# Kernel tuning notes

Measured on AMD Instinct MI355X. Metric: run time of the kernel, lower is better.

## Reference

```python
import jax, jax.numpy as jnp
import numpy as np

N = 50000          # nodes
E = 1600000        # edges (before self-loops)
DIN = 128
HEADS = (8, 8, 4)
FEATS = (16, 16, 16)
NEG_SLOPE = 0.2


def setup_inputs() -> dict:
    key = jax.random.key(0)
    ks = jax.random.split(key, 2 + 4 * 3)
    inp = {
        "X": jax.random.normal(ks[0], (N, DIN), dtype=jnp.float32),
        "A": jax.random.randint(ks[1], (2, E), 0, N, dtype=jnp.int32),
    }
    in_dims = [DIN, HEADS[0] * FEATS[0], HEADS[1] * FEATS[1]]
    k = 2
    for i, (h, f) in enumerate(zip(HEADS, FEATS)):
        din = in_dims[i]
        concat = i + 1 < len(HEADS)
        inp[f"W{i+1}"] = jax.random.normal(ks[k], (din, h * f), dtype=jnp.float32) / np.float32(np.sqrt(din)); k += 1
        inp[f"as{i+1}"] = jax.random.normal(ks[k], (h, f), dtype=jnp.float32) * 0.1; k += 1
        inp[f"ad{i+1}"] = jax.random.normal(ks[k], (h, f), dtype=jnp.float32) * 0.1; k += 1
        inp[f"b{i+1}"] = jnp.zeros((h * f if concat else f,), dtype=jnp.float32); k += 1
    return inp


def _gat_conv(x, src, dst, W, a_src, a_dst, b, concat):
    # PyG-style GATConv (eval mode, self-loops already in src/dst)
    H, F = a_src.shape
    h = (x @ W).reshape(-1, H, F)                     # [N, H, F]
    e = jax.nn.leaky_relu((h * a_src).sum(-1)[src] + (h * a_dst).sum(-1)[dst], NEG_SLOPE)  # [Etot, H]
    m = jax.ops.segment_max(e, dst, num_segments=N)   # segment softmax over dst neighborhoods
    ex = jnp.exp(e - m[dst])
    s = jax.ops.segment_sum(ex, dst, num_segments=N)
    alpha = ex / (s[dst] + 1e-16)                     # [Etot, H]
    out = jax.ops.segment_sum(h[src] * alpha[:, :, None], dst, num_segments=N)  # [N, H, F]
    out = out.reshape(N, H * F) if concat else out.mean(axis=1)
    return out + b


def reference(X, A, W1, as1, ad1, b1, W2, as2, ad2, b2, W3, as3, ad3, b3):
    loops = jnp.arange(N, dtype=A.dtype)              # GATConv default add_self_loops=True
    src = jnp.concatenate([A[0], loops])
    dst = jnp.concatenate([A[1], loops])
    x = jax.nn.relu(_gat_conv(X, src, dst, W1, as1, ad1, b1, True))
    x = jax.nn.relu(_gat_conv(x, src, dst, W2, as2, ad2, b2, True))
    return _gat_conv(x, src, dst, W3, as3, ad3, b3, False)
```

## Files before the change

kernel.cpp:

```cpp
#include <hip/hip_runtime.h>
#include <hip/hip_bf16.h>

#define NN 50000
#define EE 1600000
#define DIN 128

#define BKT_SHIFT 6
#define NB ((NN + 63) >> 6)
#define BSLACK 2688
#define CHUNK 4096

typedef _Float16 half_t;
typedef __attribute__((ext_vector_type(2))) _Float16 half2_t;
typedef __attribute__((ext_vector_type(4))) _Float16 half4_t;
typedef __attribute__((ext_vector_type(8))) _Float16 half8_t;
typedef __attribute__((ext_vector_type(4))) float float4_t;

__device__ __forceinline__ void split_write(half_t* __restrict__ bh, half_t* __restrict__ bl,
                                            int idx, float v) {
    half_t h = (half_t)v;
    bh[idx] = h;
    bl[idx] = (half_t)(v - (float)h);
}

__device__ __forceinline__ void build_bt(const float* __restrict__ W,
                                         const float* __restrict__ as,
                                         const float* __restrict__ ad,
                                         half_t* __restrict__ Bh, half_t* __restrict__ Bl,
                                         int elem, int NCOL, int H) {
    int r = elem >> 7, k = elem & 127;
    float v;
    if (r < NCOL) {
        v = W[k * NCOL + r];
    } else {
        int j = r - NCOL;
        v = 0.f;
        if (j < 8) {
            if (j < H) {
                float s = 0.f;
#pragma unroll
                for (int f = 0; f < 16; ++f) s += W[k * NCOL + j * 16 + f] * as[j * 16 + f];
                v = s;
            }
        } else {
            int hh = j - 8;
            if (hh < H) {
                float s = 0.f;
#pragma unroll
                for (int f = 0; f < 16; ++f) s += W[k * NCOL + hh * 16 + f] * ad[hh * 16 + f];
                v = s;
            }
        }
    }
    split_write(Bh, Bl, r * 128 + k, v);
}

#define T1 (144 * 128)
#define T3 (80 * 128)
__global__ __launch_bounds__(256) void prep_kernel(
    const float* __restrict__ W1, const float* __restrict__ W2, const float* __restrict__ W3,
    const float* __restrict__ as1, const float* __restrict__ ad1,
    const float* __restrict__ as2, const float* __restrict__ ad2,
    const float* __restrict__ as3, const float* __restrict__ ad3,
    half_t* __restrict__ B1h, half_t* __restrict__ B1l,
    half_t* __restrict__ B2h, half_t* __restrict__ B2l,
    half_t* __restrict__ B3h, half_t* __restrict__ B3l,
    int* __restrict__ gcursor) {
    int id = blockIdx.x * 256 + threadIdx.x;
    if (id < T1) {
        build_bt(W1, as1, ad1, B1h, B1l, id, 128, 8);
    } else if (id < 2 * T1) {
        build_bt(W2, as2, ad2, B2h, B2l, id - T1, 128, 8);
    } else if (id < 2 * T1 + T3) {
        build_bt(W3, as3, ad3, B3h, B3l, id - 2 * T1, 64, 4);
    } else {
        int i = id - (2 * T1 + T3);
        if (i < NB) gcursor[i] = 0;
    }
}

__global__ __launch_bounds__(256) void bin_kernel(const int* __restrict__ A,
                                                  int* __restrict__ gcursor,
                                                  int* __restrict__ binned, int e, int n) {
    __shared__ int lcount[NB];
    __shared__ int lbase[NB];
    int chunk0 = blockIdx.x * CHUNK;
    int cend = chunk0 + CHUNK;
    if (cend > e + n) cend = e + n;
    for (int i = threadIdx.x; i < NB; i += 256) lcount[i] = 0;
    __syncthreads();
    int sreg[16], dreg[16];
#pragma unroll
    for (int l = 0; l < 16; ++l) {
        int i = chunk0 + l * 256 + threadIdx.x;
        if (i < cend) {
            if (i < e) { sreg[l] = A[i]; dreg[l] = A[e + i]; }
            else       { sreg[l] = dreg[l] = i - e; }
            atomicAdd(&lcount[dreg[l] >> BKT_SHIFT], 1);
        } else {
            dreg[l] = -1;
        }
    }
    __syncthreads();
    for (int b = threadIdx.x; b < NB; b += 256) {
        int c = lcount[b];
        lbase[b] = c ? atomicAdd(&gcursor[b], c) : 0;
        lcount[b] = 0;
    }
    __syncthreads();
#pragma unroll
    for (int l = 0; l < 16; ++l) {
        if (dreg[l] >= 0) {
            int bkt = dreg[l] >> BKT_SHIFT;
            int pos = lbase[bkt] + atomicAdd(&lcount[bkt], 1);
            if (pos < BSLACK)
                binned[(size_t)bkt * BSLACK + pos] = (sreg[l] << 6) | (dreg[l] & 63);
        }
    }
}

__global__ __launch_bounds__(256) void fine_scatter(const int* __restrict__ binned,
                                                    const int* __restrict__ gcursor,
                                                    int* __restrict__ begE,
                                                    int* __restrict__ endE,
                                                    int* __restrict__ csr) {
    __shared__ int lc[64];
    __shared__ int scur[64];
    int b = blockIdx.x;
    int node0 = b << BKT_SHIFT;
    int cnt = gcursor[b];
    if (cnt > BSLACK) cnt = BSLACK;
    const int* bp = binned + (size_t)b * BSLACK;
    if (threadIdx.x < 64) lc[threadIdx.x] = 0;
    __syncthreads();
    for (int j = threadIdx.x; j < cnt; j += 256) atomicAdd(&lc[bp[j] & 63], 1);
    __syncthreads();
    if (threadIdx.x < 64) {
        int lane = threadIdx.x;
        int c = lc[lane];
        int v = c;
#pragma unroll
        for (int off = 1; off < 64; off <<= 1) {
            int u = __shfl_up(v, off, 64);
            if (lane >= off) v += u;
        }
        int begin = b * BSLACK + v - c;
        scur[lane] = begin;
        int node = node0 + lane;
        if (node < NN) {
            begE[node] = begin;
            endE[node] = begin + c;
        }
    }
    __syncthreads();
    for (int j = threadIdx.x; j < cnt; j += 256) {
        int v = bp[j];
        int pos = atomicAdd(&scur[v & 63], 1);
        csr[pos] = v >> 6;
    }
}

template <int NTC, int H, bool A32>
__global__ __launch_bounds__(256) void gemm_mfma(
    const float* __restrict__ X32,
    const half_t* __restrict__ Ah, const half_t* __restrict__ Al,
    const half_t* __restrict__ Bth, const half_t* __restrict__ Btl,
    half_t* __restrict__ C16, float* __restrict__ ss, float* __restrict__ ds, int M) {
    constexpr int NCOL = NTC * 16;
    constexpr int NR = NTC + 1;
    constexpr int NCHUNK = NR * 256;
    __shared__ __align__(16) half_t Bs[2][NR * 2048];
    int tid = threadIdx.x;
    int w = tid >> 6, lane = tid & 63;
    int m = lane & 15, q = lane >> 4;
    int row0 = blockIdx.x * 64 + w * 16;

    for (int P = tid; P < NCHUNK; P += 256) {
        int nt = P >> 8, k0 = (P >> 6) & 3, qq = (P >> 4) & 3, mm = P & 15;
        int src = (nt * 16 + mm) * 128 + qq * 8 + k0 * 32;
        *(half8_t*)&Bs[0][(size_t)P * 8] = *(const half8_t*)&Bth[src];
        *(half8_t*)&Bs[1][(size_t)P * 8] = *(const half8_t*)&Btl[src];
    }

    int ar = row0 + m;
    if (ar >= M) ar = M - 1;
    half8_t ahf[4], alf[4];
    if constexpr (A32) {
        const float* px = X32 + (size_t)ar * 128 + q * 8;
#pragma unroll
        for (int k0 = 0; k0 < 4; ++k0) {
            float4 u0 = *(const float4*)(px + k0 * 32);
            float4 u1 = *(const float4*)(px + k0 * 32 + 4);
            float uv[8] = {u0.x, u0.y, u0.z, u0.w, u1.x, u1.y, u1.z, u1.w};
#pragma unroll
            for (int j = 0; j < 8; ++j) {
                half_t h = (half_t)uv[j];
                ahf[k0][j] = h;
                alf[k0][j] = (half_t)(uv[j] - (float)h);
            }
        }
    } else {
        const half_t* pa = Ah + (size_t)ar * 128 + q * 8;
        const half_t* pl = Al + (size_t)ar * 128 + q * 8;
#pragma unroll
        for (int k0 = 0; k0 < 4; ++k0) {
            ahf[k0] = *(const half8_t*)(pa + k0 * 32);
            alf[k0] = *(const half8_t*)(pl + k0 * 32);
        }
    }

    __syncthreads();

    float4_t acc[NR];
#pragma unroll
    for (int nt = 0; nt < NR; ++nt) {
        acc[nt][0] = 0.f; acc[nt][1] = 0.f; acc[nt][2] = 0.f; acc[nt][3] = 0.f;
    }

#pragma unroll
    for (int nt = 0; nt < NR; ++nt) {
#pragma unroll
        for (int k0 = 0; k0 < 4; ++k0) {
            half8_t bh = *(const half8_t*)&Bs[0][(size_t)((nt * 4 + k0) * 64 + lane) * 8];
            half8_t bl = *(const half8_t*)&Bs[1][(size_t)((nt * 4 + k0) * 64 + lane) * 8];
            acc[nt] = __builtin_amdgcn_mfma_f32_16x16x32_f16(ahf[k0], bh, acc[nt], 0, 0, 0);
            acc[nt] = __builtin_amdgcn_mfma_f32_16x16x32_f16(ahf[k0], bl, acc[nt], 0, 0, 0);
            acc[nt] = __builtin_amdgcn_mfma_f32_16x16x32_f16(alf[k0], bh, acc[nt], 0, 0, 0);
        }
    }

#pragma unroll
    for (int r = 0; r < 4; ++r) {
        int grow = row0 + q * 4 + r;
        if (grow < M) {
            float v = acc[NTC][r];
            if (m < H) ss[(size_t)grow * H + m] = v;
            else if (m >= 8 && m < 8 + H) ds[(size_t)grow * H + (m - 8)] = v;
        }
    }

    __syncthreads();
    half_t* cs = (half_t*)Bs;
#pragma unroll
    for (int nt = 0; nt < NTC; ++nt)
#pragma unroll
        for (int r = 0; r < 4; ++r)
            cs[(size_t)(w * 16 + q * 4 + r) * NCOL + nt * 16 + m] = (half_t)acc[nt][r];
    constexpr int LPR = NCOL / 8;
    constexpr int RPP = 64 / LPR;
    constexpr int NP = 16 / RPP;
    int rid = lane / LPR, cid = lane % LPR;
#pragma unroll
    for (int p = 0; p < NP; ++p) {
        int r = p * RPP + rid;
        int grow = row0 + r;
        half8_t v = *(const half8_t*)&cs[(size_t)(w * 16 + r) * NCOL + cid * 8];
        if (grow < M) *(half8_t*)(C16 + (size_t)grow * NCOL + cid * 8) = v;
    }
}

template <int H, int F, bool MEAN, bool RELU>
__global__ __launch_bounds__(256) void aggregate_qw(
    const half_t* __restrict__ h, const float* __restrict__ ss, const float* __restrict__ dsc_arr,
    const int* __restrict__ csr, const int* __restrict__ begE, const int* __restrict__ endE,
    const float* __restrict__ bias, half_t* __restrict__ outh, half_t* __restrict__ outl,
    float* __restrict__ out, int n) {
    constexpr int HF = H * F;
    constexpr int FPL = HF / 16;
    int wave = blockIdx.x * (blockDim.x >> 6) + (threadIdx.x >> 6);
    int lane = threadIdx.x & 63;
    if (wave >= n) return;
    int q = lane >> 4, ql = lane & 15;
    int hf = ql * FPL;
    int hh = hf / F;
    float dsc = dsc_arr[wave * H + hh];
    int begin = begE[wave], end = endE[wave];

    float ssum = 0.f;
    float acc[FPL];
#pragma unroll
    for (int k = 0; k < FPL; ++k) acc[k] = 0.f;

    int j = begin + q;
    for (; j + 12 < end; j += 16) {
        int s0 = csr[j], s1 = csr[j + 4], s2 = csr[j + 8], s3 = csr[j + 12];
        float e0 = ss[s0 * H + hh], e1 = ss[s1 * H + hh];
        float e2 = ss[s2 * H + hh], e3 = ss[s3 * H + hh];
        const half_t* p0 = h + (size_t)s0 * HF + hf;
        const half_t* p1 = h + (size_t)s1 * HF + hf;
        const half_t* p2 = h + (size_t)s2 * HF + hf;
        const half_t* p3 = h + (size_t)s3 * HF + hf;
        e0 += dsc; e0 = (e0 > 0.f) ? e0 : 0.2f * e0;
        e1 += dsc; e1 = (e1 > 0.f) ? e1 : 0.2f * e1;
        e2 += dsc; e2 = (e2 > 0.f) ? e2 : 0.2f * e2;
        e3 += dsc; e3 = (e3 > 0.f) ? e3 : 0.2f * e3;
        float x0 = __expf(e0), x1 = __expf(e1), x2 = __expf(e2), x3 = __expf(e3);
        ssum += (x0 + x1) + (x2 + x3);
        if constexpr (FPL == 8) {
            half8_t t0 = *(const half8_t*)p0, t1 = *(const half8_t*)p1;
            half8_t t2 = *(const half8_t*)p2, t3 = *(const half8_t*)p3;
#pragma unroll
            for (int k = 0; k < 8; ++k) {
                acc[k] = fmaf(x0, (float)t0[k], acc[k]);
                acc[k] = fmaf(x1, (float)t1[k], acc[k]);
                acc[k] = fmaf(x2, (float)t2[k], acc[k]);
                acc[k] = fmaf(x3, (float)t3[k], acc[k]);
            }
        } else {
            half4_t t0 = *(const half4_t*)p0, t1 = *(const half4_t*)p1;
            half4_t t2 = *(const half4_t*)p2, t3 = *(const half4_t*)p3;
#pragma unroll
            for (int k = 0; k < 4; ++k) {
                acc[k] = fmaf(x0, (float)t0[k], acc[k]);
                acc[k] = fmaf(x1, (float)t1[k], acc[k]);
                acc[k] = fmaf(x2, (float)t2[k], acc[k]);
                acc[k] = fmaf(x3, (float)t3[k], acc[k]);
            }
        }
    }
    for (; j + 4 < end; j += 8) {
        int s0 = csr[j], s1 = csr[j + 4];
        float e0 = ss[s0 * H + hh], e1 = ss[s1 * H + hh];
        const half_t* p0 = h + (size_t)s0 * HF + hf;
        const half_t* p1 = h + (size_t)s1 * HF + hf;
        e0 += dsc; e0 = (e0 > 0.f) ? e0 : 0.2f * e0;
        e1 += dsc; e1 = (e1 > 0.f) ? e1 : 0.2f * e1;
        float x0 = __expf(e0), x1 = __expf(e1);
        ssum += x0 + x1;
        if constexpr (FPL == 8) {
            half8_t t0 = *(const half8_t*)p0, t1 = *(const half8_t*)p1;
#pragma unroll
            for (int k = 0; k < 8; ++k) {
                acc[k] = fmaf(x0, (float)t0[k], acc[k]);
                acc[k] = fmaf(x1, (float)t1[k], acc[k]);
            }
        } else {
            half4_t t0 = *(const half4_t*)p0, t1 = *(const half4_t*)p1;
#pragma unroll
            for (int k = 0; k < 4; ++k) {
                acc[k] = fmaf(x0, (float)t0[k], acc[k]);
                acc[k] = fmaf(x1, (float)t1[k], acc[k]);
            }
        }
    }
    for (; j < end; j += 4) {
        int s = csr[j];
        float e = ss[s * H + hh] + dsc;
        e = (e > 0.f) ? e : 0.2f * e;
        float x = __expf(e);
        ssum += x;
        const half_t* hp = h + (size_t)s * HF + hf;
        if constexpr (FPL == 8) {
            half8_t t = *(const half8_t*)hp;
#pragma unroll
            for (int k = 0; k < 8; ++k) acc[k] = fmaf(x, (float)t[k], acc[k]);
        } else {
            half4_t t = *(const half4_t*)hp;
#pragma unroll
            for (int k = 0; k < 4; ++k) acc[k] = fmaf(x, (float)t[k], acc[k]);
        }
    }

    ssum += __shfl_xor(ssum, 16, 64);
    ssum += __shfl_xor(ssum, 32, 64);
#pragma unroll
    for (int k = 0; k < FPL; ++k) {
        acc[k] += __shfl_xor(acc[k], 16, 64);
        acc[k] += __shfl_xor(acc[k], 32, 64);
    }

    float inv = 1.f / (ssum + 1e-16f);
    if constexpr (!MEAN) {
        if (lane < 32) {
            int k0 = (lane >> 4) * 4;
            int f = (lane & 15) * FPL + k0;
            float v[4];
#pragma unroll
            for (int i = 0; i < 4; ++i) {
                v[i] = acc[k0 + i] * inv + bias[f + i];
                if (RELU) v[i] = fmaxf(v[i], 0.f);
            }
            half4_t hh4, ll4;
#pragma unroll
            for (int i = 0; i < 4; ++i) {
                hh4[i] = (half_t)v[i];
                ll4[i] = (half_t)(v[i] - (float)hh4[i]);
            }
            *(half4_t*)(outh + (size_t)wave * HF + f) = hh4;
            *(half4_t*)(outl + (size_t)wave * HF + f) = ll4;
        }
    } else {
        float val[FPL];
#pragma unroll
        for (int k = 0; k < FPL; ++k) {
            val[k] = acc[k] * inv;
            val[k] += __shfl_xor(val[k], 4, 64);
            val[k] += __shfl_xor(val[k], 8, 64);
        }
        if (lane < 4) {
            float v0 = val[0] * 0.25f + bias[lane * 4 + 0];
            float v1 = val[1] * 0.25f + bias[lane * 4 + 1];
            float v2 = val[2] * 0.25f + bias[lane * 4 + 2];
            float v3 = val[3] * 0.25f + bias[lane * 4 + 3];
            *(float4*)(out + (size_t)wave * F + lane * 4) = make_float4(v0, v1, v2, v3);
        }
    }
}

extern "C" void kernel_launch(void* const* d_in, const int* in_sizes, int n_in,
                              void* d_out, int out_size, void* d_ws, size_t ws_size,
                              hipStream_t stream) {
    const float* X  = (const float*)d_in[0];
    const int*   A  = (const int*)d_in[1];
    const float* W1 = (const float*)d_in[2];
    const float* as1 = (const float*)d_in[3];
    const float* ad1 = (const float*)d_in[4];
    const float* b1  = (const float*)d_in[5];
    const float* W2 = (const float*)d_in[6];
    const float* as2 = (const float*)d_in[7];
    const float* ad2 = (const float*)d_in[8];
    const float* b2  = (const float*)d_in[9];
    const float* W3 = (const float*)d_in[10];
    const float* as3 = (const float*)d_in[11];
    const float* ad3 = (const float*)d_in[12];
    const float* b3  = (const float*)d_in[13];

    const int N = NN, E = EE;
    const int Etot = E + N;

    char* p = (char*)d_ws;
    auto take = [&](size_t bytes) {
        char* r = p;
        p += (bytes + 255) & ~(size_t)255;
        return (void*)r;
    };
    half_t* C16   = (half_t*)take((size_t)N * 128 * 2);
    half_t* Ph    = (half_t*)take((size_t)N * 128 * 2);
    half_t* Pl    = (half_t*)take((size_t)N * 128 * 2);
    float* ssb    = (float*)take((size_t)N * 8 * 4);
    float* dsb    = (float*)take((size_t)N * 8 * 4);
    int* begE     = (int*)take((size_t)N * 4);
    int* endE     = (int*)take((size_t)N * 4);
    int* gcursor  = (int*)take((size_t)NB * 4);
    int* csr      = (int*)take((size_t)NB * BSLACK * 4);
    half_t* B1h   = (half_t*)take(144 * 128 * 2);
    half_t* B1l   = (half_t*)take(144 * 128 * 2);
    half_t* B2h   = (half_t*)take(144 * 128 * 2);
    half_t* B2l   = (half_t*)take(144 * 128 * 2);
    half_t* B3h   = (half_t*)take(80 * 128 * 2);
    half_t* B3l   = (half_t*)take(80 * 128 * 2);
    int* binned   = (int*)Ph;

    const int prepTotal = 2 * T1 + T3 + NB;
    prep_kernel<<<(prepTotal + 255) / 256, 256, 0, stream>>>(
        W1, W2, W3, as1, ad1, as2, ad2, as3, ad3,
        B1h, B1l, B2h, B2l, B3h, B3l, gcursor);
    bin_kernel<<<(Etot + CHUNK - 1) / CHUNK, 256, 0, stream>>>(A, gcursor, binned, E, N);
    fine_scatter<<<NB, 256, 0, stream>>>(binned, gcursor, begE, endE, csr);

    const int gemmRows = (N + 63) / 64;
    const int aggBlocks = (N + 3) / 4;

    gemm_mfma<8, 8, true><<<gemmRows, 256, 0, stream>>>(X, nullptr, nullptr,
                                                        B1h, B1l, C16, ssb, dsb, N);
    aggregate_qw<8, 16, false, true>
        <<<aggBlocks, 256, 0, stream>>>(C16, ssb, dsb, csr, begE, endE, b1, Ph, Pl, nullptr, N);

    gemm_mfma<8, 8, false><<<gemmRows, 256, 0, stream>>>(nullptr, Ph, Pl,
                                                         B2h, B2l, C16, ssb, dsb, N);
    aggregate_qw<8, 16, false, true>
        <<<aggBlocks, 256, 0, stream>>>(C16, ssb, dsb, csr, begE, endE, b2, Ph, Pl, nullptr, N);

    gemm_mfma<4, 4, false><<<gemmRows, 256, 0, stream>>>(nullptr, Ph, Pl,
                                                         B3h, B3l, C16, ssb, dsb, N);
    aggregate_qw<4, 16, true, false>
        <<<aggBlocks, 256, 0, stream>>>(C16, ssb, dsb, csr, begE, endE, b3, nullptr, nullptr,
                                        (float*)d_out, N);
}
```

Baseline: 345.5 us.

## Store per-head feature planes and split aggregation by head pairs

The GEMM now writes its output as head-major planes ([head][node][16]) and the attention scores as [head][node], using a padded LDS staging tile. Aggregation is split so each block handles two heads for 16 nodes, and every gather touches only a 32-byte head slice. The aim is a smaller per-pass gather working set that fits better in L2. The cost is that edge indices are read once per head-pair pass, and the final mean now uses atomicAdd into an output that prep_kernel zeroes first.

```diff
diff --git a/kernel.cpp b/kernel.cpp
--- a/kernel.cpp
+++ b/kernel.cpp
@@ -9,6 +9,7 @@
 #define NB ((NN + 63) >> 6)
 #define BSLACK 2688
 #define CHUNK 4096
+#define ZOUT (NN * 16 / 4)
 
 typedef _Float16 half_t;
 typedef __attribute__((ext_vector_type(2))) _Float16 half2_t;
@@ -65,7 +66,7 @@
     half_t* __restrict__ B1h, half_t* __restrict__ B1l,
     half_t* __restrict__ B2h, half_t* __restrict__ B2l,
     half_t* __restrict__ B3h, half_t* __restrict__ B3l,
-    int* __restrict__ gcursor) {
+    int* __restrict__ gcursor, float* __restrict__ dout) {
     int id = blockIdx.x * 256 + threadIdx.x;
     if (id < T1) {
         build_bt(W1, as1, ad1, B1h, B1l, id, 128, 8);
@@ -75,7 +76,12 @@
         build_bt(W3, as3, ad3, B3h, B3l, id - 2 * T1, 64, 4);
     } else {
         int i = id - (2 * T1 + T3);
-        if (i < NB) gcursor[i] = 0;
+        if (i < NB) {
+            gcursor[i] = 0;
+        } else {
+            int z = i - NB;
+            if (z < ZOUT) ((float4*)dout)[z] = make_float4(0.f, 0.f, 0.f, 0.f);
+        }
     }
 }
 
@@ -234,175 +240,141 @@
         int grow = row0 + q * 4 + r;
         if (grow < M) {
             float v = acc[NTC][r];
-            if (m < H) ss[(size_t)grow * H + m] = v;
-            else if (m >= 8 && m < 8 + H) ds[(size_t)grow * H + (m - 8)] = v;
-        }
-    }
-
-    __syncthreads();
+            if (m < H) ss[(size_t)m * M + grow] = v;
+            else if (m >= 8 && m < 8 + H) ds[(size_t)(m - 8) * M + grow] = v;
+        }
+    }
+
+    __syncthreads();
+    constexpr int LDC = NCOL + 8;
     half_t* cs = (half_t*)Bs;
 #pragma unroll
     for (int nt = 0; nt < NTC; ++nt)
 #pragma unroll
         for (int r = 0; r < 4; ++r)
-            cs[(size_t)(w * 16 + q * 4 + r) * NCOL + nt * 16 + m] = (half_t)acc[nt][r];
-    constexpr int LPR = NCOL / 8;
-    constexpr int RPP = 64 / LPR;
-    constexpr int NP = 16 / RPP;
-    int rid = lane / LPR, cid = lane % LPR;
-#pragma unroll
-    for (int p = 0; p < NP; ++p) {
-        int r = p * RPP + rid;
-        int grow = row0 + r;
-        half8_t v = *(const half8_t*)&cs[(size_t)(w * 16 + r) * NCOL + cid * 8];
-        if (grow < M) *(half8_t*)(C16 + (size_t)grow * NCOL + cid * 8) = v;
-    }
-}
-
-template <int H, int F, bool MEAN, bool RELU>
-__global__ __launch_bounds__(256) void aggregate_qw(
-    const half_t* __restrict__ h, const float* __restrict__ ss, const float* __restrict__ dsc_arr,
-    const int* __restrict__ csr, const int* __restrict__ begE, const int* __restrict__ endE,
-    const float* __restrict__ bias, half_t* __restrict__ outh, half_t* __restrict__ outl,
-    float* __restrict__ out, int n) {
-    constexpr int HF = H * F;
-    constexpr int FPL = HF / 16;
-    int wave = blockIdx.x * (blockDim.x >> 6) + (threadIdx.x >> 6);
+            cs[(size_t)(w * 16 + q * 4 + r) * LDC + nt * 16 + m] = (half_t)acc[nt][r];
+    int head2 = lane >> 5, rr = (lane >> 1) & 15, hf8 = lane & 1;
+    int growc = row0 + rr;
+#pragma unroll
+    for (int p = 0; p < NTC / 2; ++p) {
+        int head = p * 2 + head2;
+        half8_t v = *(const half8_t*)&cs[(size_t)(w * 16 + rr) * LDC + head * 16 + hf8 * 8];
+        if (growc < M)
+            *(half8_t*)(C16 + ((size_t)head * M + growc) * 16 + hf8 * 8) = v;
+    }
+}
+
+template <int H, bool MEAN, bool RELU>
+__global__ __launch_bounds__(256) void aggregate_hs(
+    const half_t* __restrict__ h, const float* __restrict__ ss,
+    const float* __restrict__ dsa, const int* __restrict__ csr,
+    const int* __restrict__ begE, const int* __restrict__ endE,
+    const float* __restrict__ bias, half_t* __restrict__ outh,
+    half_t* __restrict__ outl, float* __restrict__ out, int n, int groups) {
+    int pair = blockIdx.x / groups;
+    int g = blockIdx.x - pair * groups;
     int lane = threadIdx.x & 63;
-    if (wave >= n) return;
-    int q = lane >> 4, ql = lane & 15;
-    int hf = ql * FPL;
-    int hh = hf / F;
-    float dsc = dsc_arr[wave * H + hh];
-    int begin = begE[wave], end = endE[wave];
+    int node = g * 16 + ((threadIdx.x >> 6) << 2) + (lane >> 4);
+    if (node >= n) return;
+    int ql = lane & 15;
+    int stream = ql >> 2, hh = (ql >> 1) & 1, half = ql & 1;
+    int head = pair * 2 + hh;
+    const half_t* ht = h + (size_t)head * n * 16 + half * 8;
+    const float* ssh = ss + (size_t)head * n;
+    float dsc = dsa[(size_t)head * n + node];
+    int begin = begE[node], end = endE[node];
 
     float ssum = 0.f;
-    float acc[FPL];
-#pragma unroll
-    for (int k = 0; k < FPL; ++k) acc[k] = 0.f;
-
-    int j = begin + q;
+    float acc[8];
+#pragma unroll
+    for (int k = 0; k < 8; ++k) acc[k] = 0.f;
+
+    int j = begin + stream;
     for (; j + 12 < end; j += 16) {
-        int s0 = csr[j], s1 = csr[j + 4], s2 = csr[j + 8], s3 = csr[j + 12];
-        float e0 = ss[s0 * H + hh], e1 = ss[s1 * H + hh];
-        float e2 = ss[s2 * H + hh], e3 = ss[s3 * H + hh];
-        const half_t* p0 = h + (size_t)s0 * HF + hf;
-        const half_t* p1 = h + (size_t)s1 * HF + hf;
-        const half_t* p2 = h + (size_t)s2 * HF + hf;
-        const half_t* p3 = h + (size_t)s3 * HF + hf;
-        e0 += dsc; e0 = (e0 > 0.f) ? e0 : 0.2f * e0;
-        e1 += dsc; e1 = (e1 > 0.f) ? e1 : 0.2f * e1;
-        e2 += dsc; e2 = (e2 > 0.f) ? e2 : 0.2f * e2;
-        e3 += dsc; e3 = (e3 > 0.f) ? e3 : 0.2f * e3;
+        int s0 = __builtin_nontemporal_load(&csr[j]);
+        int s1 = __builtin_nontemporal_load(&csr[j + 4]);
+        int s2 = __builtin_nontemporal_load(&csr[j + 8]);
+        int s3 = __builtin_nontemporal_load(&csr[j + 12]);
+        float e0 = ssh[s0], e1 = ssh[s1], e2 = ssh[s2], e3 = ssh[s3];
+        half8_t t0 = *(const half8_t*)(ht + (size_t)s0 * 16);
+        half8_t t1 = *(const half8_t*)(ht + (size_t)s1 * 16);
+        half8_t t2 = *(const half8_t*)(ht + (size_t)s2 * 16);
+        half8_t t3 = *(const half8_t*)(ht + (size_t)s3 * 16);
+        e0 += dsc; e1 += dsc; e2 += dsc; e3 += dsc;
+        e0 = fmaxf(e0, 0.2f * e0); e1 = fmaxf(e1, 0.2f * e1);
+        e2 = fmaxf(e2, 0.2f * e2); e3 = fmaxf(e3, 0.2f * e3);
         float x0 = __expf(e0), x1 = __expf(e1), x2 = __expf(e2), x3 = __expf(e3);
         ssum += (x0 + x1) + (x2 + x3);
-        if constexpr (FPL == 8) {
-            half8_t t0 = *(const half8_t*)p0, t1 = *(const half8_t*)p1;
-            half8_t t2 = *(const half8_t*)p2, t3 = *(const half8_t*)p3;
-#pragma unroll
-            for (int k = 0; k < 8; ++k) {
-                acc[k] = fmaf(x0, (float)t0[k], acc[k]);
-                acc[k] = fmaf(x1, (float)t1[k], acc[k]);
-                acc[k] = fmaf(x2, (float)t2[k], acc[k]);
-                acc[k] = fmaf(x3, (float)t3[k], acc[k]);
-            }
-        } else {
-            half4_t t0 = *(const half4_t*)p0, t1 = *(const half4_t*)p1;
-            half4_t t2 = *(const half4_t*)p2, t3 = *(const half4_t*)p3;
-#pragma unroll
-            for (int k = 0; k < 4; ++k) {
-                acc[k] = fmaf(x0, (float)t0[k], acc[k]);
-                acc[k] = fmaf(x1, (float)t1[k], acc[k]);
-                acc[k] = fmaf(x2, (float)t2[k], acc[k]);
-                acc[k] = fmaf(x3, (float)t3[k], acc[k]);
-            }
+#pragma unroll
+        for (int k = 0; k < 8; ++k) {
+            acc[k] = fmaf(x0, (float)t0[k], acc[k]);
+            acc[k] = fmaf(x1, (float)t1[k], acc[k]);
+            acc[k] = fmaf(x2, (float)t2[k], acc[k]);
+            acc[k] = fmaf(x3, (float)t3[k], acc[k]);
         }
     }
     for (; j + 4 < end; j += 8) {
-        int s0 = csr[j], s1 = csr[j + 4];
-        float e0 = ss[s0 * H + hh], e1 = ss[s1 * H + hh];
-        const half_t* p0 = h + (size_t)s0 * HF + hf;
-        const half_t* p1 = h + (size_t)s1 * HF + hf;
-        e0 += dsc; e0 = (e0 > 0.f) ? e0 : 0.2f * e0;
-        e1 += dsc; e1 = (e1 > 0.f) ? e1 : 0.2f * e1;
+        int s0 = __builtin_nontemporal_load(&csr[j]);
+        int s1 = __builtin_nontemporal_load(&csr[j + 4]);
+        float e0 = ssh[s0], e1 = ssh[s1];
+        half8_t t0 = *(const half8_t*)(ht + (size_t)s0 * 16);
+        half8_t t1 = *(const half8_t*)(ht + (size_t)s1 * 16);
+        e0 += dsc; e1 += dsc;
+        e0 = fmaxf(e0, 0.2f * e0); e1 = fmaxf(e1, 0.2f * e1);
         float x0 = __expf(e0), x1 = __expf(e1);
         ssum += x0 + x1;
-        if constexpr (FPL == 8) {
-            half8_t t0 = *(const half8_t*)p0, t1 = *(const half8_t*)p1;
+#pragma unroll
+        for (int k = 0; k < 8; ++k) {
+            acc[k] = fmaf(x0, (float)t0[k], acc[k]);
+            acc[k] = fmaf(x1, (float)t1[k], acc[k]);
+        }
+    }
+    for (; j < end; j += 4) {
+        int s0 = __builtin_nontemporal_load(&csr[j]);
+        float e0 = ssh[s0] + dsc;
+        half8_t t0 = *(const half8_t*)(ht + (size_t)s0 * 16);
+        e0 = fmaxf(e0, 0.2f * e0);
+        float x0 = __expf(e0);
+        ssum += x0;
+#pragma unroll
+        for (int k = 0; k < 8; ++k) acc[k] = fmaf(x0, (float)t0[k], acc[k]);
+    }
+
+    ssum += __shfl_xor(ssum, 4, 64);
+    ssum += __shfl_xor(ssum, 8, 64);
+#pragma unroll
+    for (int k = 0; k < 8; ++k) {
+        acc[k] += __shfl_xor(acc[k], 4, 64);
+        acc[k] += __shfl_xor(acc[k], 8, 64);
+    }
+    float inv = 1.f / (ssum + 1e-16f);
+
+    if constexpr (!MEAN) {
+        if (ql < 4) {
+            half8_t hv, lv;
 #pragma unroll
             for (int k = 0; k < 8; ++k) {
-                acc[k] = fmaf(x0, (float)t0[k], acc[k]);
-                acc[k] = fmaf(x1, (float)t1[k], acc[k]);
+                float t = acc[k] * inv + bias[head * 16 + half * 8 + k];
+                if (RELU) t = fmaxf(t, 0.f);
+                hv[k] = (half_t)t;
+                lv[k] = (half_t)(t - (float)hv[k]);
             }
-        } else {
-            half4_t t0 = *(const half4_t*)p0, t1 = *(const half4_t*)p1;
-#pragma unroll
-            for (int k = 0; k < 4; ++k) {
-                acc[k] = fmaf(x0, (float)t0[k], acc[k]);
-                acc[k] = fmaf(x1, (float)t1[k], acc[k]);
-            }
-        }
-    }
-    for (; j < end; j += 4) {
-        int s = csr[j];
-        float e = ss[s * H + hh] + dsc;
-        e = (e > 0.f) ? e : 0.2f * e;
-        float x = __expf(e);
-        ssum += x;
-        const half_t* hp = h + (size_t)s * HF + hf;
-        if constexpr (FPL == 8) {
-            half8_t t = *(const half8_t*)hp;
-#pragma unroll
-            for (int k = 0; k < 8; ++k) acc[k] = fmaf(x, (float)t[k], acc[k]);
-        } else {
-            half4_t t = *(const half4_t*)hp;
-#pragma unroll
-            for (int k = 0; k < 4; ++k) acc[k] = fmaf(x, (float)t[k], acc[k]);
-        }
-    }
-
-    ssum += __shfl_xor(ssum, 16, 64);
-    ssum += __shfl_xor(ssum, 32, 64);
-#pragma unroll
-    for (int k = 0; k < FPL; ++k) {
-        acc[k] += __shfl_xor(acc[k], 16, 64);
-        acc[k] += __shfl_xor(acc[k], 32, 64);
-    }
-
-    float inv = 1.f / (ssum + 1e-16f);
-    if constexpr (!MEAN) {
-        if (lane < 32) {
-            int k0 = (lane >> 4) * 4;
-            int f = (lane & 15) * FPL + k0;
-            float v[4];
-#pragma unroll
-            for (int i = 0; i < 4; ++i) {
-                v[i] = acc[k0 + i] * inv + bias[f + i];
-                if (RELU) v[i] = fmaxf(v[i], 0.f);
-            }
-            half4_t hh4, ll4;
-#pragma unroll
-            for (int i = 0; i < 4; ++i) {
-                hh4[i] = (half_t)v[i];
-                ll4[i] = (half_t)(v[i] - (float)hh4[i]);
-            }
-            *(half4_t*)(outh + (size_t)wave * HF + f) = hh4;
-            *(half4_t*)(outl + (size_t)wave * HF + f) = ll4;
+            size_t off = (size_t)node * (H * 16) + head * 16 + half * 8;
+            *(half8_t*)(outh + off) = hv;
+            *(half8_t*)(outl + off) = lv;
         }
     } else {
-        float val[FPL];
-#pragma unroll
-        for (int k = 0; k < FPL; ++k) {
-            val[k] = acc[k] * inv;
-            val[k] += __shfl_xor(val[k], 4, 64);
-            val[k] += __shfl_xor(val[k], 8, 64);
-        }
-        if (lane < 4) {
-            float v0 = val[0] * 0.25f + bias[lane * 4 + 0];
-            float v1 = val[1] * 0.25f + bias[lane * 4 + 1];
-            float v2 = val[2] * 0.25f + bias[lane * 4 + 2];
-            float v3 = val[3] * 0.25f + bias[lane * 4 + 3];
-            *(float4*)(out + (size_t)wave * F + lane * 4) = make_float4(v0, v1, v2, v3);
+        float v[8];
+#pragma unroll
+        for (int k = 0; k < 8; ++k) {
+            float t = acc[k] * inv;
+            t += __shfl_xor(t, 2, 64);
+            v[k] = t * 0.25f + bias[half * 8 + k] * 0.5f;
+        }
+        if (ql < 2) {
+#pragma unroll
+            for (int k = 0; k < 8; ++k)
+                atomicAdd(out + (size_t)node * 16 + half * 8 + k, v[k]);
         }
     }
 }
@@ -451,29 +423,28 @@
     half_t* B3l   = (half_t*)take(80 * 128 * 2);
     int* binned   = (int*)Ph;
 
-    const int prepTotal = 2 * T1 + T3 + NB;
+    const int prepTotal = 2 * T1 + T3 + NB + ZOUT;
     prep_kernel<<<(prepTotal + 255) / 256, 256, 0, stream>>>(
         W1, W2, W3, as1, ad1, as2, ad2, as3, ad3,
-        B1h, B1l, B2h, B2l, B3h, B3l, gcursor);
+        B1h, B1l, B2h, B2l, B3h, B3l, gcursor, (float*)d_out);
     bin_kernel<<<(Etot + CHUNK - 1) / CHUNK, 256, 0, stream>>>(A, gcursor, binned, E, N);
     fine_scatter<<<NB, 256, 0, stream>>>(binned, gcursor, begE, endE, csr);
 
     const int gemmRows = (N + 63) / 64;
-    const int aggBlocks = (N + 3) / 4;
+    const int aggGroups = (N + 15) / 16;
 
     gemm_mfma<8, 8, true><<<gemmRows, 256, 0, stream>>>(X, nullptr, nullptr,
                                                         B1h, B1l, C16, ssb, dsb, N);
-    aggregate_qw<8, 16, false, true>
-        <<<aggBlocks, 256, 0, stream>>>(C16, ssb, dsb, csr, begE, endE, b1, Ph, Pl, nullptr, N);
+    aggregate_hs<8, false, true><<<aggGroups * 4, 256, 0, stream>>>(
+        C16, ssb, dsb, csr, begE, endE, b1, Ph, Pl, nullptr, N, aggGroups);
 
     gemm_mfma<8, 8, false><<<gemmRows, 256, 0, stream>>>(nullptr, Ph, Pl,
                                                          B2h, B2l, C16, ssb, dsb, N);
-    aggregate_qw<8, 16, false, true>
-        <<<aggBlocks, 256, 0, stream>>>(C16, ssb, dsb, csr, begE, endE, b2, Ph, Pl, nullptr, N);
+    aggregate_hs<8, false, true><<<aggGroups * 4, 256, 0, stream>>>(
+        C16, ssb, dsb, csr, begE, endE, b2, Ph, Pl, nullptr, N, aggGroups);
 
     gemm_mfma<4, 4, false><<<gemmRows, 256, 0, stream>>>(nullptr, Ph, Pl,
                                                          B3h, B3l, C16, ssb, dsb, N);
-    aggregate_qw<4, 16, true, false>
-        <<<aggBlocks, 256, 0, stream>>>(C16, ssb, dsb, csr, begE, endE, b3, nullptr, nullptr,
-                                        (float*)d_out, N);
-}
+    aggregate_hs<4, true, false><<<aggGroups * 2, 256, 0, stream>>>(
+        C16, ssb, dsb, csr, begE, endE, b3, nullptr, nullptr, (float*)d_out, N, aggGroups);
+}
```

After: 592.9 us. +71.6%, slower.
